# Kernel tuning notes

Hardware: AMD Instinct MI355X
Metric: run time of the kernel (lower is better)

The kernel has to match this reference:

```python
import jax, jax.numpy as jnp
import numpy as np

N, IN_DIM, H1, H2, HEADS = 3072, 256, 128, 64, 4
NEG_INF = -9.0e15  # matches torch zero_vec = -9e15

def _xavier(key, shape):
    fan_in, fan_out = shape[-2], shape[-1]
    lim = np.sqrt(6.0 / (fan_in + fan_out)).astype(np.float32)
    return jax.random.uniform(key, shape, jnp.float32, -lim, lim)

def setup_inputs() -> dict:
    key = jax.random.key(0)
    ks = jax.random.split(key, 14)
    x = jax.random.normal(ks[0], (N, IN_DIM), jnp.float32)
    adj = jax.random.randint(ks[1], (N, N), 0, 2, jnp.int32)
    # layer 1 params (per-head stacked)
    W1 = _xavier(ks[2], (HEADS, IN_DIM, H1))
    a1s = _xavier(ks[3], (HEADS, H1)) * 1.414   # a[:F] of the (2F,1) xavier vector
    a1d = _xavier(ks[4], (HEADS, H1)) * 1.414   # a[F:]
    lin1 = _xavier(ks[5], (HEADS * H1, H1))
    res1 = _xavier(ks[6], (IN_DIM, H1))
    # layer 2 params
    W2 = _xavier(ks[7], (HEADS, H1, H2))
    a2s = _xavier(ks[8], (HEADS, H2)) * 1.414
    a2d = _xavier(ks[9], (HEADS, H2)) * 1.414
    lin2 = _xavier(ks[10], (HEADS * H2, H2))
    res2 = _xavier(ks[11], (H1, H2))
    return {"x": x, "adj": adj, "W1": W1, "a1s": a1s, "a1d": a1d,
            "lin1": lin1, "res1": res1, "W2": W2, "a2s": a2s, "a2d": a2d,
            "lin2": lin2, "res2": res2}

def _gat_residual_layer(h, mask, W, a_s, a_d, lin, res):
    # h: [N, F_in], W: [H, F_in, F_out], mask: [N, N] bool
    Wh = jnp.einsum('nf,hfo->hno', h, W)                 # [H, N, F_out]
    src = jnp.einsum('hno,ho->hn', Wh, a_s)              # Wh @ a[:F]
    dst = jnp.einsum('hno,ho->hn', Wh, a_d)              # Wh @ a[F:]
    e = src[:, :, None] + dst[:, None, :]                # [H, N, N]
    e = jnp.where(e > 0, e, 0.2 * e)                     # leaky_relu(0.2)
    e = jnp.where(mask[None], e, NEG_INF)                # adj mask
    attn = jax.nn.softmax(e, axis=-1)                    # dropout p=0.1 -> identity (eval)
    hp = jax.nn.elu(jnp.einsum('hij,hjo->hio', attn, Wh))  # per-head output, elu
    n = h.shape[0]
    hp = jnp.transpose(hp, (1, 0, 2)).reshape(n, -1)     # concat heads (head-major)
    hp = jax.nn.elu(hp @ lin)                            # multi-head mix + elu
    out = jax.nn.relu(hp + h @ res)                      # residual + relu
    return jax.nn.relu(out)                              # encoder-loop relu; dropout(0.4) identity

def reference(x, adj, W1, a1s, a1d, lin1, res1, W2, a2s, a2d, lin2, res2):
    mask = adj > 0
    h = _gat_residual_layer(x, mask, W1, a1s, a1d, lin1, res1)
    h = _gat_residual_layer(h, mask, W2, a2s, a2d, lin2, res2)
    return h  # embedding [N, H2]
```

## Files before the change

kernel.cpp:

```cpp
#include <hip/hip_runtime.h>
#include <hip/hip_bf16.h>
#include <stdint.h>

using bf16 = __hip_bfloat16;
typedef short short8 __attribute__((ext_vector_type(8)));
typedef short short4v __attribute__((ext_vector_type(4)));
typedef float f32x4 __attribute__((ext_vector_type(4)));
typedef uint32_t u32x4 __attribute__((ext_vector_type(4)));

constexpr int N = 3072;
constexpr int D0 = 256;
constexpr int F1 = 128;
constexpr int F2 = 64;
constexpr int HEADS = 4;
constexpr int NW = N / 32;
constexpr float CSHIFT = 20.0f;

#define DI __device__ __forceinline__
DI short f2bs(float v) { bf16 b = __float2bfloat16(v); return *(short*)&b; }

__global__ __launch_bounds__(256) void k_pack_adj(const int* __restrict__ adj,
                                                  uint32_t* __restrict__ bits) {
  int idx = blockIdx.x * 256 + threadIdx.x;
  unsigned long long m = __ballot(adj[idx] > 0);
  if ((threadIdx.x & 63) == 0) {
    bits[idx >> 5]       = (uint32_t)m;
    bits[(idx >> 5) + 1] = (uint32_t)(m >> 32);
  }
}

__global__ __launch_bounds__(256) void k_cvt(const float* __restrict__ x,
                                             const float* __restrict__ W1,
                                             const float* __restrict__ lin1,
                                             const float* __restrict__ res1,
                                             const float* __restrict__ W2,
                                             const float* __restrict__ lin2,
                                             const float* __restrict__ res2,
                                             bf16* __restrict__ xb,
                                             bf16* __restrict__ W1T,
                                             bf16* __restrict__ lin1T,
                                             bf16* __restrict__ res1T,
                                             bf16* __restrict__ W2T,
                                             bf16* __restrict__ lin2T,
                                             bf16* __restrict__ res2T) {
  int t = blockIdx.y;
  int i = blockIdx.x * 256 + threadIdx.x;
  switch (t) {
    case 0:
      if (i < N * D0) xb[i] = __float2bfloat16(x[i]);
      break;
    case 1:
      if (i < HEADS * F1 * D0) { int k = i & 255; int ho = i >> 8; int h = ho >> 7, o = ho & 127;
        W1T[i] = __float2bfloat16(W1[((size_t)h * D0 + k) * F1 + o]); }
      break;
    case 2:
      if (i < F1 * HEADS * F1) { int k = i & 511; int o = i >> 9;
        lin1T[i] = __float2bfloat16(lin1[k * F1 + o]); }
      break;
    case 3:
      if (i < F1 * D0) { int k = i & 255; int o = i >> 8;
        res1T[i] = __float2bfloat16(res1[k * F1 + o]); }
      break;
    case 4:
      if (i < HEADS * F2 * F1) { int k = i & 127; int ho = i >> 7; int h = ho >> 6, o = ho & 63;
        W2T[i] = __float2bfloat16(W2[((size_t)h * F1 + k) * F2 + o]); }
      break;
    case 5:
      if (i < F2 * HEADS * F2) { int k = i & 255; int o = i >> 8;
        lin2T[i] = __float2bfloat16(lin2[k * F2 + o]); }
      break;
    case 6:
      if (i < F2 * F1) { int k = i & 127; int o = i >> 7;
        res2T[i] = __float2bfloat16(res2[k * F2 + o]); }
      break;
  }
}

template <int K, int NOUT, int F>
__global__ __launch_bounds__(256) void k_whead_mfma(const bf16* __restrict__ A,
                                                    const bf16* __restrict__ BT,
                                                    bf16* __restrict__ WhT,
                                                    const float* __restrict__ as_,
                                                    const float* __restrict__ ad_,
                                                    float* __restrict__ src,
                                                    float* __restrict__ dst) {
  int row0 = blockIdx.x * 16;
  int wid = threadIdx.x >> 6, lane = threadIdx.x & 63;
  int l15 = lane & 15, q = lane >> 4;
  int col = blockIdx.y * 64 + wid * 16 + l15;

  const bf16* aP = A + (size_t)(row0 + l15) * K + q * 8;
  const bf16* bP = BT + (size_t)col * K + q * 8;
  f32x4 acc;
#pragma unroll
  for (int r = 0; r < 4; r++) acc[r] = 0.f;
#pragma unroll
  for (int ks = 0; ks < K / 32; ks++) {
    short8 a = *(const short8*)(aP + ks * 32);
    short8 b = *(const short8*)(bP + ks * 32);
    acc = __builtin_amdgcn_mfma_f32_16x16x32_bf16(a, b, acc, 0, 0, 0);
  }

  short4v w;
#pragma unroll
  for (int r = 0; r < 4; r++) w[r] = f2bs(acc[r]);
  *(short4v*)(WhT + (size_t)col * N + row0 + q * 4) = w;

  int h = col / F;
  float asv = as_[col], adv = ad_[col];
#pragma unroll
  for (int r = 0; r < 4; r++) {
    float sp = acc[r] * asv, dp = acc[r] * adv;
#pragma unroll
    for (int m = 1; m < 16; m <<= 1) {
      sp += __shfl_xor(sp, m);
      dp += __shfl_xor(dp, m);
    }
    if (l15 == 0) {
      atomicAdd(&src[h * N + row0 + q * 4 + r], sp);
      atomicAdd(&dst[h * N + row0 + q * 4 + r], dp);
    }
  }
}

template <int F, int CSPLIT>
__global__ __launch_bounds__(256) void k_attn_fused(const bf16* __restrict__ WhT,
                                                    const float* __restrict__ src,
                                                    const float* __restrict__ dst,
                                                    const uint32_t* __restrict__ bits,
                                                    bf16* __restrict__ hp) {
  constexpr int FL = F / CSPLIT;
  constexpr int CT = FL / 16;
  constexpr int JT = 128;
  constexpr int NT = N / JT;
  constexpr int STG = FL * JT * 2 / (256 * 16);
  int h   = blockIdx.y / CSPLIT;
  int cs  = blockIdx.y % CSPLIT;
  int cb  = h * F + cs * FL;
  int i0  = blockIdx.x * 64;
  int tid = threadIdx.x, wid = tid >> 6, lane = tid & 63;
  int l15 = lane & 15, q = lane >> 4;
  int row = i0 + wid * 16 + l15;

  __shared__ float sDst[N];
  __shared__ __align__(16) char sB[2][FL * JT * 2];

  for (int t = tid; t < N; t += 256) sDst[t] = dst[h * N + t];
  float srcr = src[h * N + row];
  const uint32_t* brow = bits + (size_t)row * NW;

  const bf16* gsrc[STG];
  int ldst[STG];
#pragma unroll
  for (int c = 0; c < STG; c++) {
    int fb  = c * 4096 + tid * 16;
    int col = fb >> 8, jb = (fb & 255) >> 4;
    gsrc[c] = WhT + (size_t)(cb + col) * N + jb * 8;
    ldst[c] = col * 256 + ((jb * 16) ^ ((col & 15) << 4));
  }

  f32x4 acc[CT];
#pragma unroll
  for (int ct = 0; ct < CT; ct++)
#pragma unroll
    for (int r = 0; r < 4; r++) acc[ct][r] = 0.f;
  float rowsum = 0.f;

  short8 rg[STG];
#pragma unroll
  for (int c = 0; c < STG; c++) rg[c] = *(const short8*)(gsrc[c]);
#pragma unroll
  for (int c = 0; c < STG; c++) *(short8*)(&sB[0][ldst[c]]) = rg[c];

  for (int t = 0; t < NT; t++) {
    __syncthreads();
    if (t + 1 < NT) {
#pragma unroll
      for (int c = 0; c < STG; c++) rg[c] = *(const short8*)(gsrc[c] + (size_t)(t + 1) * JT);
    }
    u32x4 wds = *(const u32x4*)(brow + t * 4);
    const char* bb = sB[t & 1];
#pragma unroll
    for (int ks = 0; ks < 4; ks++) {
      const f32x4* dp = (const f32x4*)(&sDst[t * JT + ks * 32 + q * 8]);
      f32x4 dlo = dp[0], dhi = dp[1];
      uint32_t myb = (wds[ks] >> (q * 8)) & 0xffu;
      float pv[8];
#pragma unroll
      for (int e = 0; e < 8; e++) {
        float tv = srcr + (e < 4 ? dlo[e] : dhi[e - 4]);
        tv = tv > 0.f ? tv : 0.2f * tv;
        float pe = ((myb >> e) & 1u) ? __expf(tv - CSHIFT) : 0.f;
        rowsum += pe;
        pv[e] = pe;
      }
      short8 a;
#pragma unroll
      for (int e = 0; e < 8; e++) a[e] = f2bs(pv[e]);
#pragma unroll
      for (int ct = 0; ct < CT; ct++) {
        int col = ct * 16 + l15;
        short8 b = *(const short8*)(bb + col * 256 + (((ks * 4 + q) << 4) ^ (l15 << 4)));
        acc[ct] = __builtin_amdgcn_mfma_f32_16x16x32_bf16(a, b, acc[ct], 0, 0, 0);
      }
    }
    __syncthreads();
    if (t + 1 < NT) {
#pragma unroll
      for (int c = 0; c < STG; c++) *(short8*)(&sB[(t + 1) & 1][ldst[c]]) = rg[c];
    }
  }

  rowsum += __shfl_xor(rowsum, 16);
  rowsum += __shfl_xor(rowsum, 32);

#pragma unroll
  for (int ct = 0; ct < CT; ct++)
#pragma unroll
    for (int r = 0; r < 4; r++) {
      float rs = __shfl(rowsum, q * 4 + r);
      float v  = acc[ct][r] / rs;
      v = v > 0.f ? v : __expf(v) - 1.f;
      int gi = i0 + wid * 16 + q * 4 + r;
      hp[(size_t)gi * (HEADS * F) + h * F + cs * FL + ct * 16 + l15] = __float2bfloat16(v);
    }
}

template <int K1, int K2, int NOUT, bool F32OUT>
__global__ __launch_bounds__(256) void k_mix_mfma(const bf16* __restrict__ A1,
                                                  const bf16* __restrict__ B1T,
                                                  const bf16* __restrict__ A2,
                                                  const bf16* __restrict__ B2T,
                                                  void* __restrict__ outv) {
  int row0 = blockIdx.x * 16;
  int wid = threadIdx.x >> 6, lane = threadIdx.x & 63;
  int l15 = lane & 15, q = lane >> 4;
  int col = blockIdx.y * 64 + wid * 16 + l15;

  f32x4 acc1, acc2;
#pragma unroll
  for (int r = 0; r < 4; r++) { acc1[r] = 0.f; acc2[r] = 0.f; }

  const bf16* a1P = A1 + (size_t)(row0 + l15) * K1 + q * 8;
  const bf16* b1P = B1T + (size_t)col * K1 + q * 8;
#pragma unroll
  for (int ks = 0; ks < K1 / 32; ks++) {
    short8 a = *(const short8*)(a1P + ks * 32);
    short8 b = *(const short8*)(b1P + ks * 32);
    acc1 = __builtin_amdgcn_mfma_f32_16x16x32_bf16(a, b, acc1, 0, 0, 0);
  }
  const bf16* a2P = A2 + (size_t)(row0 + l15) * K2 + q * 8;
  const bf16* b2P = B2T + (size_t)col * K2 + q * 8;
#pragma unroll
  for (int ks = 0; ks < K2 / 32; ks++) {
    short8 a = *(const short8*)(a2P + ks * 32);
    short8 b = *(const short8*)(b2P + ks * 32);
    acc2 = __builtin_amdgcn_mfma_f32_16x16x32_bf16(a, b, acc2, 0, 0, 0);
  }

#pragma unroll
  for (int r = 0; r < 4; r++) {
    float v = acc1[r];
    v = v > 0.f ? v : __expf(v) - 1.f;
    v += acc2[r];
    v = v > 0.f ? v : 0.f;
    int rw = row0 + q * 4 + r;
    if (F32OUT) ((float*)outv)[(size_t)rw * NOUT + col] = v;
    else        ((bf16*)outv)[(size_t)rw * NOUT + col] = __float2bfloat16(v);
  }
}

extern "C" void kernel_launch(void* const* d_in, const int* in_sizes, int n_in,
                              void* d_out, int out_size, void* d_ws, size_t ws_size,
                              hipStream_t stream) {
  const float* x    = (const float*)d_in[0];
  const int*   adj  = (const int*)d_in[1];
  const float* W1   = (const float*)d_in[2];
  const float* a1s  = (const float*)d_in[3];
  const float* a1d  = (const float*)d_in[4];
  const float* lin1 = (const float*)d_in[5];
  const float* res1 = (const float*)d_in[6];
  const float* W2   = (const float*)d_in[7];
  const float* a2s  = (const float*)d_in[8];
  const float* a2d  = (const float*)d_in[9];
  const float* lin2 = (const float*)d_in[10];
  const float* res2 = (const float*)d_in[11];
  float* out = (float*)d_out;

  char* p = (char*)d_ws;
  auto alloc = [&](size_t bytes) { void* r = (void*)p; p += (bytes + 255) & ~(size_t)255; return r; };
  uint32_t* bits = (uint32_t*)alloc((size_t)N * NW * 4);
  bf16* xb    = (bf16*)alloc((size_t)N * D0 * 2);
  bf16* W1T   = (bf16*)alloc((size_t)HEADS * F1 * D0 * 2);
  bf16* lin1T = (bf16*)alloc((size_t)F1 * HEADS * F1 * 2);
  bf16* res1T = (bf16*)alloc((size_t)F1 * D0 * 2);
  bf16* W2T   = (bf16*)alloc((size_t)HEADS * F2 * F1 * 2);
  bf16* lin2T = (bf16*)alloc((size_t)F2 * HEADS * F2 * 2);
  bf16* res2T = (bf16*)alloc((size_t)F2 * F1 * 2);
  bf16* WhT1  = (bf16*)alloc((size_t)HEADS * F1 * N * 2);
  bf16* WhT2  = (bf16*)alloc((size_t)HEADS * F2 * N * 2);
  float* src1 = (float*)alloc((size_t)HEADS * N * 4);
  float* dst1 = (float*)alloc((size_t)HEADS * N * 4);
  float* src2 = (float*)alloc((size_t)HEADS * N * 4);
  float* dst2 = (float*)alloc((size_t)HEADS * N * 4);
  bf16* hp1   = (bf16*)alloc((size_t)N * HEADS * F1 * 2);
  bf16* hp2   = (bf16*)alloc((size_t)N * HEADS * F2 * 2);
  bf16* h1b   = (bf16*)alloc((size_t)N * F1 * 2);

  hipMemsetAsync(src1, 0, (size_t)HEADS * N * 4 * 4, stream);

  k_pack_adj<<<dim3(N * N / 256), dim3(256), 0, stream>>>(adj, bits);
  k_cvt<<<dim3(N * D0 / 256, 7), dim3(256), 0, stream>>>(x, W1, lin1, res1, W2, lin2, res2,
                                                         xb, W1T, lin1T, res1T, W2T, lin2T, res2T);

  k_whead_mfma<D0, HEADS * F1, F1>
      <<<dim3(N / 16, HEADS * F1 / 64), dim3(256), 0, stream>>>(xb, W1T, WhT1, a1s, a1d, src1, dst1);
  k_attn_fused<F1, 2><<<dim3(N / 64, HEADS * 2), dim3(256), 0, stream>>>(WhT1, src1, dst1, bits, hp1);
  k_mix_mfma<HEADS * F1, D0, F1, false>
      <<<dim3(N / 16, F1 / 64), dim3(256), 0, stream>>>(hp1, lin1T, xb, res1T, h1b);

  k_whead_mfma<F1, HEADS * F2, F2>
      <<<dim3(N / 16, HEADS * F2 / 64), dim3(256), 0, stream>>>(h1b, W2T, WhT2, a2s, a2d, src2, dst2);
  k_attn_fused<F2, 2><<<dim3(N / 64, HEADS * 2), dim3(256), 0, stream>>>(WhT2, src2, dst2, bits, hp2);
  k_mix_mfma<HEADS * F2, F1, F2, true>
      <<<dim3(N / 16, F2 / 64), dim3(256), 0, stream>>>(hp2, lin2T, h1b, res2T, out);
}
```

Measured before the change: 261.1 us.

## Prepack Wh into MFMA fragment layout and split attention over key halves

The Wh projection now writes its output directly in the per-lane MFMA B-fragment order. The attention kernel can then load B operands straight from global memory, which removes the shared-memory staging and double buffering. Attention work is split across the key dimension: each block handles 32 rows and each wave takes its own chunk of 384 keys. Per-wave partial sums are reduced in LDS and written as fp32 partials with atomic row sums, and a new combine kernel does the normalization and ELU. This raises parallelism and B-operand reuse across two row tiles. The cost is extra fp32 partial traffic, atomics and an added launch.

```diff
diff --git a/kernel.cpp b/kernel.cpp
--- a/kernel.cpp
+++ b/kernel.cpp
@@ -6,7 +6,6 @@
 typedef short short8 __attribute__((ext_vector_type(8)));
 typedef short short4v __attribute__((ext_vector_type(4)));
 typedef float f32x4 __attribute__((ext_vector_type(4)));
-typedef uint32_t u32x4 __attribute__((ext_vector_type(4)));
 
 constexpr int N = 3072;
 constexpr int D0 = 256;
@@ -79,7 +78,7 @@
 template <int K, int NOUT, int F>
 __global__ __launch_bounds__(256) void k_whead_mfma(const bf16* __restrict__ A,
                                                     const bf16* __restrict__ BT,
-                                                    bf16* __restrict__ WhT,
+                                                    bf16* __restrict__ BP,
                                                     const float* __restrict__ as_,
                                                     const float* __restrict__ ad_,
                                                     float* __restrict__ src,
@@ -101,12 +100,18 @@
     acc = __builtin_amdgcn_mfma_f32_16x16x32_bf16(a, b, acc, 0, 0, 0);
   }
 
+  int h  = col / F;
+  int cl = col % F;
+  int ct = cl >> 4;
+  int jt = row0 >> 5;
+  int qp = ((row0 >> 4) & 1) * 2 + (q >> 1);
+  int eo = (q & 1) * 4;
   short4v w;
 #pragma unroll
   for (int r = 0; r < 4; r++) w[r] = f2bs(acc[r]);
-  *(short4v*)(WhT + (size_t)col * N + row0 + q * 4) = w;
-
-  int h = col / F;
+  size_t off = ((((size_t)h * (F / 16) + ct) * (N / 32) + jt) * 4 + qp) * 128 + l15 * 8 + eo;
+  *(short4v*)(BP + off) = w;
+
   float asv = as_[col], adv = ad_[col];
 #pragma unroll
   for (int r = 0; r < 4; r++) {
@@ -123,107 +128,114 @@
   }
 }
 
-template <int F, int CSPLIT>
-__global__ __launch_bounds__(256) void k_attn_fused(const bf16* __restrict__ WhT,
-                                                    const float* __restrict__ src,
-                                                    const float* __restrict__ dst,
-                                                    const uint32_t* __restrict__ bits,
-                                                    bf16* __restrict__ hp) {
-  constexpr int FL = F / CSPLIT;
-  constexpr int CT = FL / 16;
-  constexpr int JT = 128;
-  constexpr int NT = N / JT;
-  constexpr int STG = FL * JT * 2 / (256 * 16);
-  int h   = blockIdx.y / CSPLIT;
-  int cs  = blockIdx.y % CSPLIT;
-  int cb  = h * F + cs * FL;
-  int i0  = blockIdx.x * 64;
+template <int F>
+__global__ __launch_bounds__(256, 2) void k_attn_fused(const bf16* __restrict__ BP,
+                                                       const float* __restrict__ src,
+                                                       const float* __restrict__ dst,
+                                                       const uint32_t* __restrict__ bits,
+                                                       float* __restrict__ hp_part,
+                                                       float* __restrict__ rs_part) {
+  constexpr int CT = F / 16;
+  constexpr int CTN = CT / 4;
+  constexpr int KSTEPS = 12;
+  int h    = blockIdx.y;
+  int kb   = blockIdx.z;
+  int row0 = blockIdx.x * 32;
   int tid = threadIdx.x, wid = tid >> 6, lane = tid & 63;
   int l15 = lane & 15, q = lane >> 4;
-  int row = i0 + wid * 16 + l15;
-
-  __shared__ float sDst[N];
-  __shared__ __align__(16) char sB[2][FL * JT * 2];
-
-  for (int t = tid; t < N; t += 256) sDst[t] = dst[h * N + t];
-  float srcr = src[h * N + row];
-  const uint32_t* brow = bits + (size_t)row * NW;
-
-  const bf16* gsrc[STG];
-  int ldst[STG];
-#pragma unroll
-  for (int c = 0; c < STG; c++) {
-    int fb  = c * 4096 + tid * 16;
-    int col = fb >> 8, jb = (fb & 255) >> 4;
-    gsrc[c] = WhT + (size_t)(cb + col) * N + jb * 8;
-    ldst[c] = col * 256 + ((jb * 16) ^ ((col & 15) << 4));
-  }
-
-  f32x4 acc[CT];
+  int jbase = kb * (N / 2) + wid * 384;
+
+  float src0 = src[h * N + row0 + l15];
+  float src1 = src[h * N + row0 + 16 + l15];
+  const float* dh = dst + h * N;
+  const uint32_t* b0 = bits + (size_t)(row0 + l15) * NW;
+  const uint32_t* b1 = bits + (size_t)(row0 + 16 + l15) * NW;
+  const bf16* bph = BP + (size_t)h * CT * (N / 32) * 512;
+
+  f32x4 acc0[CT], acc1[CT];
 #pragma unroll
   for (int ct = 0; ct < CT; ct++)
 #pragma unroll
-    for (int r = 0; r < 4; r++) acc[ct][r] = 0.f;
-  float rowsum = 0.f;
-
-  short8 rg[STG];
-#pragma unroll
-  for (int c = 0; c < STG; c++) rg[c] = *(const short8*)(gsrc[c]);
-#pragma unroll
-  for (int c = 0; c < STG; c++) *(short8*)(&sB[0][ldst[c]]) = rg[c];
-
-  for (int t = 0; t < NT; t++) {
+    for (int r = 0; r < 4; r++) { acc0[ct][r] = 0.f; acc1[ct][r] = 0.f; }
+  float rs0 = 0.f, rs1 = 0.f;
+
+  for (int ks = 0; ks < KSTEPS; ks++) {
+    int j0 = jbase + ks * 32;
+    int jt = j0 >> 5;
+    f32x4 dlo = *(const f32x4*)(dh + j0 + q * 8);
+    f32x4 dhi = *(const f32x4*)(dh + j0 + q * 8 + 4);
+    uint32_t m0 = (b0[jt] >> (q * 8)) & 0xffu;
+    uint32_t m1 = (b1[jt] >> (q * 8)) & 0xffu;
+    float pv0[8], pv1[8];
+#pragma unroll
+    for (int e = 0; e < 8; e++) {
+      float d = e < 4 ? dlo[e] : dhi[e - 4];
+      float t0 = src0 + d; t0 = fmaxf(t0, 0.2f * t0);
+      float p0 = ((m0 >> e) & 1u) ? __expf(t0 - CSHIFT) : 0.f;
+      rs0 += p0; pv0[e] = p0;
+      float t1 = src1 + d; t1 = fmaxf(t1, 0.2f * t1);
+      float p1 = ((m1 >> e) & 1u) ? __expf(t1 - CSHIFT) : 0.f;
+      rs1 += p1; pv1[e] = p1;
+    }
+    short8 a0, a1;
+#pragma unroll
+    for (int e = 0; e < 8; e++) { a0[e] = f2bs(pv0[e]); a1[e] = f2bs(pv1[e]); }
+#pragma unroll
+    for (int ct = 0; ct < CT; ct++) {
+      short8 b = *(const short8*)(bph + (((size_t)ct * (N / 32) + jt) * 64 + lane) * 8);
+      acc0[ct] = __builtin_amdgcn_mfma_f32_16x16x32_bf16(a0, b, acc0[ct], 0, 0, 0);
+      acc1[ct] = __builtin_amdgcn_mfma_f32_16x16x32_bf16(a1, b, acc1[ct], 0, 0, 0);
+    }
+  }
+
+  rs0 += __shfl_xor(rs0, 16); rs0 += __shfl_xor(rs0, 32);
+  rs1 += __shfl_xor(rs1, 16); rs1 += __shfl_xor(rs1, 32);
+  if (q == 0) atomicAdd(&rs_part[((size_t)kb * HEADS + h) * N + row0 + l15], rs0);
+  if (q == 1) atomicAdd(&rs_part[((size_t)kb * HEADS + h) * N + row0 + 16 + l15], rs1);
+
+  __shared__ float red[4][64][CT * 4 + 1];
+#pragma unroll
+  for (int t = 0; t < 2; t++) {
     __syncthreads();
-    if (t + 1 < NT) {
-#pragma unroll
-      for (int c = 0; c < STG; c++) rg[c] = *(const short8*)(gsrc[c] + (size_t)(t + 1) * JT);
-    }
-    u32x4 wds = *(const u32x4*)(brow + t * 4);
-    const char* bb = sB[t & 1];
-#pragma unroll
-    for (int ks = 0; ks < 4; ks++) {
-      const f32x4* dp = (const f32x4*)(&sDst[t * JT + ks * 32 + q * 8]);
-      f32x4 dlo = dp[0], dhi = dp[1];
-      uint32_t myb = (wds[ks] >> (q * 8)) & 0xffu;
-      float pv[8];
-#pragma unroll
-      for (int e = 0; e < 8; e++) {
-        float tv = srcr + (e < 4 ? dlo[e] : dhi[e - 4]);
-        tv = tv > 0.f ? tv : 0.2f * tv;
-        float pe = ((myb >> e) & 1u) ? __expf(tv - CSHIFT) : 0.f;
-        rowsum += pe;
-        pv[e] = pe;
+#pragma unroll
+    for (int ct = 0; ct < CT; ct++)
+#pragma unroll
+      for (int r = 0; r < 4; r++)
+        red[wid][lane][ct * 4 + r] = t ? acc1[ct][r] : acc0[ct][r];
+    __syncthreads();
+#pragma unroll
+    for (int cc = 0; cc < CTN; cc++) {
+      int ct = wid * CTN + cc;
+#pragma unroll
+      for (int r = 0; r < 4; r++) {
+        float v = red[0][lane][ct * 4 + r] + red[1][lane][ct * 4 + r] +
+                  red[2][lane][ct * 4 + r] + red[3][lane][ct * 4 + r];
+        int row = row0 + t * 16 + q * 4 + r;
+        hp_part[((size_t)kb * N + row) * (HEADS * F) + h * F + ct * 16 + l15] = v;
       }
-      short8 a;
-#pragma unroll
-      for (int e = 0; e < 8; e++) a[e] = f2bs(pv[e]);
-#pragma unroll
-      for (int ct = 0; ct < CT; ct++) {
-        int col = ct * 16 + l15;
-        short8 b = *(const short8*)(bb + col * 256 + (((ks * 4 + q) << 4) ^ (l15 << 4)));
-        acc[ct] = __builtin_amdgcn_mfma_f32_16x16x32_bf16(a, b, acc[ct], 0, 0, 0);
-      }
-    }
-    __syncthreads();
-    if (t + 1 < NT) {
-#pragma unroll
-      for (int c = 0; c < STG; c++) *(short8*)(&sB[(t + 1) & 1][ldst[c]]) = rg[c];
-    }
-  }
-
-  rowsum += __shfl_xor(rowsum, 16);
-  rowsum += __shfl_xor(rowsum, 32);
-
-#pragma unroll
-  for (int ct = 0; ct < CT; ct++)
-#pragma unroll
-    for (int r = 0; r < 4; r++) {
-      float rs = __shfl(rowsum, q * 4 + r);
-      float v  = acc[ct][r] / rs;
-      v = v > 0.f ? v : __expf(v) - 1.f;
-      int gi = i0 + wid * 16 + q * 4 + r;
-      hp[(size_t)gi * (HEADS * F) + h * F + cs * FL + ct * 16 + l15] = __float2bfloat16(v);
-    }
+    }
+  }
+}
+
+template <int F>
+__global__ __launch_bounds__(256) void k_attn_combine(const float* __restrict__ hp_part,
+                                                      const float* __restrict__ rs_part,
+                                                      bf16* __restrict__ hp) {
+  constexpr int HF = HEADS * F;
+  int i = (blockIdx.x * 256 + threadIdx.x) * 4;
+  int row = i / HF, c = i % HF, h = c / F;
+  f32x4 p0 = *(const f32x4*)(hp_part + (size_t)row * HF + c);
+  f32x4 p1 = *(const f32x4*)(hp_part + ((size_t)N + row) * HF + c);
+  float s = rs_part[h * N + row] + rs_part[(HEADS + h) * N + row];
+  float inv = 1.f / s;
+  short4v o;
+#pragma unroll
+  for (int r = 0; r < 4; r++) {
+    float v = (p0[r] + p1[r]) * inv;
+    v = v > 0.f ? v : __expf(v) - 1.f;
+    o[r] = f2bs(v);
+  }
+  *(short4v*)(hp + i) = o;
 }
 
 template <int K1, int K2, int NOUT, bool F32OUT>
@@ -297,31 +309,37 @@
   bf16* W2T   = (bf16*)alloc((size_t)HEADS * F2 * F1 * 2);
   bf16* lin2T = (bf16*)alloc((size_t)F2 * HEADS * F2 * 2);
   bf16* res2T = (bf16*)alloc((size_t)F2 * F1 * 2);
-  bf16* WhT1  = (bf16*)alloc((size_t)HEADS * F1 * N * 2);
-  bf16* WhT2  = (bf16*)alloc((size_t)HEADS * F2 * N * 2);
+  bf16* BP1   = (bf16*)alloc((size_t)HEADS * F1 * N * 2);
+  bf16* BP2   = (bf16*)alloc((size_t)HEADS * F2 * N * 2);
   float* src1 = (float*)alloc((size_t)HEADS * N * 4);
   float* dst1 = (float*)alloc((size_t)HEADS * N * 4);
   float* src2 = (float*)alloc((size_t)HEADS * N * 4);
   float* dst2 = (float*)alloc((size_t)HEADS * N * 4);
+  float* rs1  = (float*)alloc((size_t)2 * HEADS * N * 4);
+  float* rs2  = (float*)alloc((size_t)2 * HEADS * N * 4);
+  float* hpp1 = (float*)alloc((size_t)2 * N * HEADS * F1 * 4);
+  float* hpp2 = (float*)alloc((size_t)2 * N * HEADS * F2 * 4);
   bf16* hp1   = (bf16*)alloc((size_t)N * HEADS * F1 * 2);
   bf16* hp2   = (bf16*)alloc((size_t)N * HEADS * F2 * 2);
   bf16* h1b   = (bf16*)alloc((size_t)N * F1 * 2);
 
-  hipMemsetAsync(src1, 0, (size_t)HEADS * N * 4 * 4, stream);
+  hipMemsetAsync(src1, 0, (size_t)HEADS * N * 4 * 8, stream);
 
   k_pack_adj<<<dim3(N * N / 256), dim3(256), 0, stream>>>(adj, bits);
   k_cvt<<<dim3(N * D0 / 256, 7), dim3(256), 0, stream>>>(x, W1, lin1, res1, W2, lin2, res2,
                                                          xb, W1T, lin1T, res1T, W2T, lin2T, res2T);
 
   k_whead_mfma<D0, HEADS * F1, F1>
-      <<<dim3(N / 16, HEADS * F1 / 64), dim3(256), 0, stream>>>(xb, W1T, WhT1, a1s, a1d, src1, dst1);
-  k_attn_fused<F1, 2><<<dim3(N / 64, HEADS * 2), dim3(256), 0, stream>>>(WhT1, src1, dst1, bits, hp1);
+      <<<dim3(N / 16, HEADS * F1 / 64), dim3(256), 0, stream>>>(xb, W1T, BP1, a1s, a1d, src1, dst1);
+  k_attn_fused<F1><<<dim3(N / 32, HEADS, 2), dim3(256), 0, stream>>>(BP1, src1, dst1, bits, hpp1, rs1);
+  k_attn_combine<F1><<<dim3(N * HEADS * F1 / 1024), dim3(256), 0, stream>>>(hpp1, rs1, hp1);
   k_mix_mfma<HEADS * F1, D0, F1, false>
       <<<dim3(N / 16, F1 / 64), dim3(256), 0, stream>>>(hp1, lin1T, xb, res1T, h1b);
 
   k_whead_mfma<F1, HEADS * F2, F2>
-      <<<dim3(N / 16, HEADS * F2 / 64), dim3(256), 0, stream>>>(h1b, W2T, WhT2, a2s, a2d, src2, dst2);
-  k_attn_fused<F2, 2><<<dim3(N / 64, HEADS * 2), dim3(256), 0, stream>>>(WhT2, src2, dst2, bits, hp2);
+      <<<dim3(N / 16, HEADS * F2 / 64), dim3(256), 0, stream>>>(h1b, W2T, BP2, a2s, a2d, src2, dst2);
+  k_attn_fused<F2><<<dim3(N / 32, HEADS, 2), dim3(256), 0, stream>>>(BP2, src2, dst2, bits, hpp2, rs2);
+  k_attn_combine<F2><<<dim3(N * HEADS * F2 / 1024), dim3(256), 0, stream>>>(hpp2, rs2, hp2);
   k_mix_mfma<HEADS * F2, F1, F2, true>
       <<<dim3(N / 16, F2 / 64), dim3(256), 0, stream>>>(hp2, lin2T, h1b, res2T, out);
 }
```

After: 208.9 us. 1.25x faster.
